# Optimization experiments

Hardware: AMD Instinct MI355X
Metric: run time of the kernel (lower is better)

Reference implementation:

```python
import jax, jax.numpy as jnp
import numpy as np


def setup_inputs() -> dict:
    key = jax.random.key(0)
    k1, k2, k3, k4 = jax.random.split(key, 4)
    B, S, H = 4, 2048, 1024
    Ha, P = 1024, 1024
    x = jax.random.normal(k1, (B, S, H), dtype=jnp.float32)
    score_weights = jax.random.normal(k2, (B, S, S), dtype=jnp.float32)
    W_c = jax.random.normal(k3, (H, 3 * Ha), dtype=jnp.float32) * 0.02
    b_c = jnp.zeros((3 * Ha,), dtype=jnp.float32)
    W_p = jax.random.normal(k4, (Ha, P), dtype=jnp.float32) * 0.02
    b_p = jnp.zeros((P,), dtype=jnp.float32)
    return {"x": x, "score_weights": score_weights, "W_c": W_c, "b_c": b_c, "W_p": W_p, "b_p": b_p}


def reference(x, score_weights, W_c, b_c, W_p, b_p):
    # fused QKV projection: [B,S,H] @ [H,3*Ha] + b -> [B,S,3*Ha]
    c = jnp.einsum("bsh,hf->bsf", x, W_c) + b_c
    Ha = c.shape[-1] // 3
    query, key, value = jnp.split(c, 3, axis=2)  # each [B,S,Ha]
    # scaled dot-product scores [B,S,S] with additive bias
    scale = jax.lax.rsqrt(jnp.asarray(Ha, dtype=x.dtype))
    scores = jnp.einsum("bqd,bkd->bqk", query, key) * scale + score_weights
    probs = jax.nn.softmax(scores, axis=-1)
    context = jnp.einsum("bqk,bkd->bqd", probs, value)  # [B,S,Ha]
    # output projection [B,S,Ha] @ [Ha,P] + b -> [B,S,P]
    return jnp.einsum("bsd,dp->bsp", context, W_p) + b_p
```

## Files before the change

### kernel.cpp

```cpp
#include <hip/hip_runtime.h>
#include <hip/hip_bf16.h>
#include <cstdint>

typedef __attribute__((ext_vector_type(8))) short v8s;
typedef __attribute__((ext_vector_type(4))) float v4f;

__device__ __forceinline__ unsigned short f32_to_bf16(float f) {
  unsigned int u = __builtin_bit_cast(unsigned int, f);
  u += 0x7fffu + ((u >> 16) & 1u);
  return (unsigned short)(u >> 16);
}

__device__ __forceinline__ void gload_lds16(const void* g, void* l) {
  __builtin_amdgcn_global_load_lds((const __attribute__((address_space(1))) void*)g,
                                   (__attribute__((address_space(3))) void*)l, 16, 0, 0);
}

enum { EPI_BF16_BIAS = 0, EPI_F32_BIAS = 1, EPI_F32_SCALE_ADD = 2 };

template <int MODE>
__global__ __launch_bounds__(256)
void gemm_nt(const unsigned short* __restrict__ A, long long strideA, int lda,
             const unsigned short* __restrict__ B, long long strideB, int ldb,
             void* __restrict__ Cout, long long strideC, int ldc,
             const float* __restrict__ bias,
             const float* __restrict__ addmat, long long strideAdd,
             float scale, int K,
             unsigned short* __restrict__ VtOut)
{
  __shared__ __attribute__((aligned(16))) short smA[2][128 * 64];
  __shared__ __attribute__((aligned(16))) short smB[2][128 * 64];

  const int tid  = threadIdx.x;
  const int lane = tid & 63;
  const int wave = tid >> 6;
  const int wm = wave >> 1, wn = wave & 1;
  const int bz = blockIdx.z;
  const int tileM = blockIdx.y * 128, tileN = blockIdx.x * 128;

  const unsigned short* Ag = A + (long long)bz * strideA + (long long)tileM * lda;
  const unsigned short* Bg = B + (long long)bz * strideB + (long long)tileN * ldb;

  const int l8    = lane >> 3;
  const int srcCb = (lane & 7) ^ l8;

  v4f acc[4][4] = {};
  const int nt = K >> 6;

#define STAGE128(buf, t) do { \
    _Pragma("unroll") \
    for (int i_ = 0; i_ < 4; ++i_) { \
      const int c_   = wave * 4 + i_; \
      const int row_ = c_ * 8 + l8; \
      gload_lds16(Ag + (long long)row_ * lda + (long long)(t) * 64 + srcCb * 8, \
                  &smA[buf][c_ * 512]); \
      gload_lds16(Bg + (long long)row_ * ldb + (long long)(t) * 64 + srcCb * 8, \
                  &smB[buf][c_ * 512]); \
    } \
  } while (0)

  STAGE128(0, 0);
  __syncthreads();

  for (int t = 0; t < nt; ++t) {
    const int cur = t & 1;
    if (t + 1 < nt) STAGE128(cur ^ 1, t + 1);
    #pragma unroll
    for (int kk = 0; kk < 2; ++kk) {
      v8s af[4], bf[4];
      #pragma unroll
      for (int f = 0; f < 4; ++f) {
        const int rA = wm * 64 + f * 16 + (lane & 15);
        const int cA = (kk * 4 + (lane >> 4)) ^ (rA & 7);
        af[f] = *(const v8s*)&smA[cur][rA * 64 + cA * 8];
        const int rB = wn * 64 + f * 16 + (lane & 15);
        const int cB = (kk * 4 + (lane >> 4)) ^ (rB & 7);
        bf[f] = *(const v8s*)&smB[cur][rB * 64 + cB * 8];
      }
      #pragma unroll
      for (int fm = 0; fm < 4; ++fm)
        #pragma unroll
        for (int fn = 0; fn < 4; ++fn)
          acc[fm][fn] = __builtin_amdgcn_mfma_f32_16x16x32_bf16(af[fm], bf[fn], acc[fm][fn], 0, 0, 0);
    }
    __syncthreads();
  }
#undef STAGE128

  const int row0 = tileM + wm * 64 + (lane >> 4) * 4;
  const int col0 = tileN + wn * 64 + (lane & 15);
  const bool vtActive = (MODE == EPI_BF16_BIAS) && (VtOut != nullptr) && (tileN >= 2048);

  #pragma unroll
  for (int fm = 0; fm < 4; ++fm) {
    #pragma unroll
    for (int fn = 0; fn < 4; ++fn) {
      const int col = col0 + fn * 16;
      if (vtActive) {
        const int rowb = row0 + fm * 16;
        const int d = col - 2048;
        const int b = rowb >> 11;
        const int s0 = rowb & 2047;
        const float bb = bias[col];
        ushort4 w;
        w.x = f32_to_bf16(acc[fm][fn][0] + bb);
        w.y = f32_to_bf16(acc[fm][fn][1] + bb);
        w.z = f32_to_bf16(acc[fm][fn][2] + bb);
        w.w = f32_to_bf16(acc[fm][fn][3] + bb);
        *(ushort4*)&VtOut[((long long)b * 1024 + d) * 2048 + s0] = w;
      } else {
        #pragma unroll
        for (int r = 0; r < 4; ++r) {
          const int row = row0 + fm * 16 + r;
          const float v = acc[fm][fn][r];
          if (MODE == EPI_F32_SCALE_ADD) {
            float* C = (float*)Cout + (long long)bz * strideC;
            const float* Wt = addmat + (long long)bz * strideAdd;
            C[(long long)row * ldc + col] = v * scale + Wt[(long long)row * ldc + col];
          } else if (MODE == EPI_F32_BIAS) {
            float* C = (float*)Cout + (long long)bz * strideC;
            C[(long long)row * ldc + col] = v + bias[col];
          } else {
            unsigned short* C = (unsigned short*)Cout + (long long)bz * strideC;
            const float b = bias ? bias[col] : 0.0f;
            C[(long long)row * ldc + col] = f32_to_bf16(v + b);
          }
        }
      }
    }
  }
}

__global__ __launch_bounds__(256)
void cvt_f32_bf16_kernel(const float* __restrict__ in, unsigned short* __restrict__ out,
                         long long n)
{
  const long long i = ((long long)blockIdx.x * 256 + threadIdx.x) * 4;
  if (i >= n) return;
  const float4 v = *(const float4*)(in + i);
  typedef __attribute__((ext_vector_type(4))) unsigned short v4us;
  v4us o;
  o.x = f32_to_bf16(v.x); o.y = f32_to_bf16(v.y);
  o.z = f32_to_bf16(v.z); o.w = f32_to_bf16(v.w);
  *(v4us*)(out + i) = o;
}

__global__ __launch_bounds__(256)
void transpose_f32_bf16_kernel(const float* __restrict__ in, unsigned short* __restrict__ out,
                               int R, int C)
{
  __shared__ float t[32][33];
  const int c0 = blockIdx.x * 32, r0 = blockIdx.y * 32;
  const int tx = threadIdx.x, ty = threadIdx.y;
  for (int i = ty; i < 32; i += 8)
    t[i][tx] = in[(long long)(r0 + i) * C + (c0 + tx)];
  __syncthreads();
  for (int i = ty; i < 32; i += 8)
    out[(long long)(c0 + i) * R + (r0 + tx)] = f32_to_bf16(t[tx][i]);
}

__global__ __launch_bounds__(256)
void softmax_rows(const float* __restrict__ scores, unsigned short* __restrict__ probs)
{
  const long long row = blockIdx.x;
  const float* src = scores + row * 2048;
  unsigned short* dst = probs + row * 2048;
  const int t = threadIdx.x;
  float v[8];
  const float4 a = *(const float4*)(src + t * 8);
  const float4 b = *(const float4*)(src + t * 8 + 4);
  v[0]=a.x; v[1]=a.y; v[2]=a.z; v[3]=a.w; v[4]=b.x; v[5]=b.y; v[6]=b.z; v[7]=b.w;

  float m = v[0];
  #pragma unroll
  for (int j = 1; j < 8; ++j) m = fmaxf(m, v[j]);
  for (int o = 32; o; o >>= 1) m = fmaxf(m, __shfl_xor(m, o));
  __shared__ float redm[4], reds[4];
  if ((t & 63) == 0) redm[t >> 6] = m;
  __syncthreads();
  m = fmaxf(fmaxf(redm[0], redm[1]), fmaxf(redm[2], redm[3]));

  float s = 0.f;
  #pragma unroll
  for (int j = 0; j < 8; ++j) { v[j] = __expf(v[j] - m); s += v[j]; }
  for (int o = 32; o; o >>= 1) s += __shfl_xor(s, o);
  if ((t & 63) == 0) reds[t >> 6] = s;
  __syncthreads();
  s = reds[0] + reds[1] + reds[2] + reds[3];
  const float inv = 1.0f / s;

  v8s o8;
  #pragma unroll
  for (int j = 0; j < 8; ++j) o8[j] = (short)f32_to_bf16(v[j] * inv);
  *(v8s*)(dst + t * 8) = o8;
}

extern "C" void kernel_launch(void* const* d_in, const int* in_sizes, int n_in,
                              void* d_out, int out_size, void* d_ws, size_t ws_size,
                              hipStream_t stream) {
  (void)in_sizes; (void)n_in; (void)out_size; (void)ws_size;
  const float* x   = (const float*)d_in[0];
  const float* sw  = (const float*)d_in[1];
  const float* W_c = (const float*)d_in[2];
  const float* b_c = (const float*)d_in[3];
  const float* W_p = (const float*)d_in[4];
  const float* b_p = (const float*)d_in[5];
  float* out = (float*)d_out;

  const int Bb = 4, S = 2048, H = 1024, Ha = 1024, P = 1024;
  const int M = Bb * S;
  char* ws = (char*)d_ws;
  const long long MB = 1024LL * 1024LL;
  float*          scores = (float*)(ws + 0);
  unsigned short* x_bf   = (unsigned short*)(ws + 0);
  unsigned short* ctx    = (unsigned short*)(ws + 0);
  unsigned short* probs  = (unsigned short*)(ws + 64 * MB);
  unsigned short* qkv    = (unsigned short*)(ws + 96 * MB);
  unsigned short* Vt     = (unsigned short*)(ws + 144 * MB);
  unsigned short* Wc_t   = (unsigned short*)(ws + 160 * MB);
  unsigned short* Wp_t   = (unsigned short*)(ws + 166 * MB);

  const dim3 tb(32, 8);

  cvt_f32_bf16_kernel<<<(unsigned)((long long)M * H / 4 / 256), 256, 0, stream>>>(
      x, x_bf, (long long)M * H);
  transpose_f32_bf16_kernel<<<dim3(3 * Ha / 32, H / 32), tb, 0, stream>>>(W_c, Wc_t, H, 3 * Ha);
  transpose_f32_bf16_kernel<<<dim3(P / 32, Ha / 32), tb, 0, stream>>>(W_p, Wp_t, Ha, P);
  gemm_nt<EPI_BF16_BIAS><<<dim3(3 * Ha / 128, M / 128, 1), 256, 0, stream>>>(
      x_bf, 0, H, Wc_t, 0, H, qkv, 0, 3 * Ha, b_c, nullptr, 0, 0.f, H, Vt);
  gemm_nt<EPI_F32_SCALE_ADD><<<dim3(S / 128, S / 128, Bb), 256, 0, stream>>>(
      qkv, (long long)S * 3 * Ha, 3 * Ha,
      qkv + Ha, (long long)S * 3 * Ha, 3 * Ha,
      scores, (long long)S * S, S, nullptr, sw, (long long)S * S, 0.03125f, Ha, nullptr);
  softmax_rows<<<Bb * S, 256, 0, stream>>>(scores, probs);
  gemm_nt<EPI_BF16_BIAS><<<dim3(Ha / 128, S / 128, Bb), 256, 0, stream>>>(
      probs, (long long)S * S, S, Vt, (long long)Ha * S, S,
      ctx, (long long)S * Ha, Ha, nullptr, nullptr, 0, 0.f, S, nullptr);
  gemm_nt<EPI_F32_BIAS><<<dim3(P / 128, M / 128, 1), 256, 0, stream>>>(
      ctx, 0, Ha, Wp_t, 0, Ha, out, 0, P, b_p, nullptr, 0, 0.f, Ha, nullptr);
}
```

Before: 253.3 us.

## Switch GEMM to 32x32x16 MFMA and drop LDS double buffering

Replaces the 16x16x32 bf16 MFMA tiling (4x4 fragments per wave) with 32x32x16 MFMAs (2x2 fragments per wave), cutting LDS fragment reads per FLOP. It also removes the double-buffered async global->LDS prefetch in favour of a single buffer with load, sync, compute, sync. Halving LDS may raise occupancy, but global load latency is no longer overlapped with compute, which risks stalls.

```diff
diff --git a/kernel.cpp b/kernel.cpp
--- a/kernel.cpp
+++ b/kernel.cpp
@@ -3,7 +3,7 @@
 #include <cstdint>
 
 typedef __attribute__((ext_vector_type(8))) short v8s;
-typedef __attribute__((ext_vector_type(4))) float v4f;
+typedef __attribute__((ext_vector_type(16))) float v16f;
 
 __device__ __forceinline__ unsigned short f32_to_bf16(float f) {
   unsigned int u = __builtin_bit_cast(unsigned int, f);
@@ -28,8 +28,8 @@
              float scale, int K,
              unsigned short* __restrict__ VtOut)
 {
-  __shared__ __attribute__((aligned(16))) short smA[2][128 * 64];
-  __shared__ __attribute__((aligned(16))) short smB[2][128 * 64];
+  __shared__ __attribute__((aligned(16))) short smA[128 * 64];
+  __shared__ __attribute__((aligned(16))) short smB[128 * 64];
 
   const int tid  = threadIdx.x;
   const int lane = tid & 63;
@@ -43,87 +43,78 @@
 
   const int l8    = lane >> 3;
   const int srcCb = (lane & 7) ^ l8;
-
-  v4f acc[4][4] = {};
-  const int nt = K >> 6;
-
-#define STAGE128(buf, t) do { \
-    _Pragma("unroll") \
-    for (int i_ = 0; i_ < 4; ++i_) { \
-      const int c_   = wave * 4 + i_; \
-      const int row_ = c_ * 8 + l8; \
-      gload_lds16(Ag + (long long)row_ * lda + (long long)(t) * 64 + srcCb * 8, \
-                  &smA[buf][c_ * 512]); \
-      gload_lds16(Bg + (long long)row_ * ldb + (long long)(t) * 64 + srcCb * 8, \
-                  &smB[buf][c_ * 512]); \
-    } \
-  } while (0)
-
-  STAGE128(0, 0);
-  __syncthreads();
-
-  for (int t = 0; t < nt; ++t) {
-    const int cur = t & 1;
-    if (t + 1 < nt) STAGE128(cur ^ 1, t + 1);
+  const int l31   = lane & 31, l5 = lane >> 5;
+
+  v16f acc[2][2] = {};
+
+  const int rA0 = wm * 64 + l31;
+  const int rB0 = wn * 64 + l31;
+  const int swzRow = l31 & 7;
+
+  for (int k0 = 0; k0 < K; k0 += 64) {
     #pragma unroll
-    for (int kk = 0; kk < 2; ++kk) {
-      v8s af[4], bf[4];
-      #pragma unroll
-      for (int f = 0; f < 4; ++f) {
-        const int rA = wm * 64 + f * 16 + (lane & 15);
-        const int cA = (kk * 4 + (lane >> 4)) ^ (rA & 7);
-        af[f] = *(const v8s*)&smA[cur][rA * 64 + cA * 8];
-        const int rB = wn * 64 + f * 16 + (lane & 15);
-        const int cB = (kk * 4 + (lane >> 4)) ^ (rB & 7);
-        bf[f] = *(const v8s*)&smB[cur][rB * 64 + cB * 8];
-      }
-      #pragma unroll
-      for (int fm = 0; fm < 4; ++fm)
-        #pragma unroll
-        for (int fn = 0; fn < 4; ++fn)
-          acc[fm][fn] = __builtin_amdgcn_mfma_f32_16x16x32_bf16(af[fm], bf[fn], acc[fm][fn], 0, 0, 0);
+    for (int i = 0; i < 4; ++i) {
+      const int c   = wave * 4 + i;
+      const int row = c * 8 + l8;
+      gload_lds16(Ag + (long long)row * lda + k0 + srcCb * 8, &smA[c * 512]);
+      gload_lds16(Bg + (long long)row * ldb + k0 + srcCb * 8, &smB[c * 512]);
+    }
+    __syncthreads();
+    #pragma unroll
+    for (int ks = 0; ks < 4; ++ks) {
+      const int cb = (ks * 2 + l5) ^ swzRow;
+      const v8s a0 = *(const v8s*)&smA[rA0 * 64 + cb * 8];
+      const v8s a1 = *(const v8s*)&smA[(rA0 + 32) * 64 + cb * 8];
+      const v8s b0 = *(const v8s*)&smB[rB0 * 64 + cb * 8];
+      const v8s b1 = *(const v8s*)&smB[(rB0 + 32) * 64 + cb * 8];
+      acc[0][0] = __builtin_amdgcn_mfma_f32_32x32x16_bf16(a0, b0, acc[0][0], 0, 0, 0);
+      acc[0][1] = __builtin_amdgcn_mfma_f32_32x32x16_bf16(a0, b1, acc[0][1], 0, 0, 0);
+      acc[1][0] = __builtin_amdgcn_mfma_f32_32x32x16_bf16(a1, b0, acc[1][0], 0, 0, 0);
+      acc[1][1] = __builtin_amdgcn_mfma_f32_32x32x16_bf16(a1, b1, acc[1][1], 0, 0, 0);
     }
     __syncthreads();
   }
-#undef STAGE128
-
-  const int row0 = tileM + wm * 64 + (lane >> 4) * 4;
-  const int col0 = tileN + wn * 64 + (lane & 15);
+
+  const int row0 = tileM + wm * 64 + l5 * 4;
+  const int col0 = tileN + wn * 64 + l31;
   const bool vtActive = (MODE == EPI_BF16_BIAS) && (VtOut != nullptr) && (tileN >= 2048);
 
   #pragma unroll
-  for (int fm = 0; fm < 4; ++fm) {
+  for (int mi = 0; mi < 2; ++mi) {
     #pragma unroll
-    for (int fn = 0; fn < 4; ++fn) {
-      const int col = col0 + fn * 16;
-      if (vtActive) {
-        const int rowb = row0 + fm * 16;
-        const int d = col - 2048;
-        const int b = rowb >> 11;
-        const int s0 = rowb & 2047;
-        const float bb = bias[col];
-        ushort4 w;
-        w.x = f32_to_bf16(acc[fm][fn][0] + bb);
-        w.y = f32_to_bf16(acc[fm][fn][1] + bb);
-        w.z = f32_to_bf16(acc[fm][fn][2] + bb);
-        w.w = f32_to_bf16(acc[fm][fn][3] + bb);
-        *(ushort4*)&VtOut[((long long)b * 1024 + d) * 2048 + s0] = w;
-      } else {
-        #pragma unroll
-        for (int r = 0; r < 4; ++r) {
-          const int row = row0 + fm * 16 + r;
-          const float v = acc[fm][fn][r];
-          if (MODE == EPI_F32_SCALE_ADD) {
-            float* C = (float*)Cout + (long long)bz * strideC;
-            const float* Wt = addmat + (long long)bz * strideAdd;
-            C[(long long)row * ldc + col] = v * scale + Wt[(long long)row * ldc + col];
-          } else if (MODE == EPI_F32_BIAS) {
-            float* C = (float*)Cout + (long long)bz * strideC;
-            C[(long long)row * ldc + col] = v + bias[col];
-          } else {
-            unsigned short* C = (unsigned short*)Cout + (long long)bz * strideC;
-            const float b = bias ? bias[col] : 0.0f;
-            C[(long long)row * ldc + col] = f32_to_bf16(v + b);
+    for (int ni = 0; ni < 2; ++ni) {
+      const int col = col0 + ni * 32;
+      #pragma unroll
+      for (int qg = 0; qg < 4; ++qg) {
+        const int rowb = row0 + mi * 32 + qg * 8;
+        if (vtActive) {
+          const int d  = col - 2048;
+          const int b  = rowb >> 11;
+          const int s0 = rowb & 2047;
+          const float bb = bias[col];
+          ushort4 w;
+          w.x = f32_to_bf16(acc[mi][ni][qg * 4 + 0] + bb);
+          w.y = f32_to_bf16(acc[mi][ni][qg * 4 + 1] + bb);
+          w.z = f32_to_bf16(acc[mi][ni][qg * 4 + 2] + bb);
+          w.w = f32_to_bf16(acc[mi][ni][qg * 4 + 3] + bb);
+          *(ushort4*)&VtOut[((long long)b * 1024 + d) * 2048 + s0] = w;
+        } else {
+          #pragma unroll
+          for (int j = 0; j < 4; ++j) {
+            const int row = rowb + j;
+            const float v = acc[mi][ni][qg * 4 + j];
+            if (MODE == EPI_F32_SCALE_ADD) {
+              float* C = (float*)Cout + (long long)bz * strideC;
+              const float* Wt = addmat + (long long)bz * strideAdd;
+              C[(long long)row * ldc + col] = v * scale + Wt[(long long)row * ldc + col];
+            } else if (MODE == EPI_F32_BIAS) {
+              float* C = (float*)Cout + (long long)bz * strideC;
+              C[(long long)row * ldc + col] = v + bias[col];
+            } else {
+              unsigned short* C = (unsigned short*)Cout + (long long)bz * strideC;
+              const float b = bias ? bias[col] : 0.0f;
+              C[(long long)row * ldc + col] = f32_to_bf16(v + b);
+            }
           }
         }
       }
```

After: 256.8 us. No clear change (+1.4%).
